# Kernel tuning notes

Hardware: AMD Instinct MI355X
Metric: run time of the kernel (lower is better)

Reference implementation:

```python
import jax, jax.numpy as jnp
import numpy as np

N_NODES = 256


def _lstm_layer(x, W, b):
    # x: [B, T, D]; W: [D+H, 4H]; b: [4H]. TF BasicLSTMCell, forget_bias=1.0,
    # gate order (i, j, f, o).
    B, T, D = x.shape
    H = N_NODES

    def step(carry, xt):
        c, h = carry
        gates = jnp.dot(jnp.concatenate([xt, h], axis=1), W) + b  # [B, 4H]
        i, j, f, o = jnp.split(gates, 4, axis=1)
        c_new = c * jax.nn.sigmoid(f + 1.0) + jax.nn.sigmoid(i) * jnp.tanh(j)
        h_new = jnp.tanh(c_new) * jax.nn.sigmoid(o)
        return (c_new, h_new), h_new

    init = (jnp.zeros((B, H), x.dtype), jnp.zeros((B, H), x.dtype))
    _, ys = jax.lax.scan(step, init, jnp.swapaxes(x, 0, 1))  # ys: [T, B, H]
    return jnp.swapaxes(ys, 0, 1)


def setup_inputs() -> dict:
    key = jax.random.key(0)
    k_x, k_w0, k_w1 = jax.random.split(key, 3)
    B, T, D, H = 32, 2048, 256, N_NODES
    x = jax.random.normal(k_x, (B, T, D), dtype=jnp.float32)
    W0 = jax.random.normal(k_w0, (D + H, 4 * H), dtype=jnp.float32) * 0.05
    b0 = jnp.zeros((4 * H,), dtype=jnp.float32)
    W1 = jax.random.normal(k_w1, (H + H, 4 * H), dtype=jnp.float32) * 0.05
    b1 = jnp.zeros((4 * H,), dtype=jnp.float32)
    return {"x": x, "W0": W0, "b0": b0, "W1": W1, "b1": b1}


def reference(x, W0, b0, W1, b1):
    # 2-layer LSTM stack, zero initial states, keepProb=1.0 (no dropout).
    h = _lstm_layer(x, W0, b0)
    h = _lstm_layer(h, W1, b1)
    # activations = reshape(outputs, [-1, nNodes * numCells]), numCells = 1
    return h.reshape(-1, N_NODES)
```

## Files before the change

### kernel.cpp

```cpp
#include <hip/hip_runtime.h>
#include <hip/hip_bf16.h>
#include <hip/hip_fp16.h>


typedef _Float16 half_t;
typedef __attribute__((ext_vector_type(2))) _Float16 h2v;

static __device__ __forceinline__ float bf2f(unsigned short u) {
  union { unsigned u; float f; } v; v.u = ((unsigned)u) << 16; return v.f;
}
static __device__ __forceinline__ unsigned short f2bf(float f) {
  union { float f; unsigned u; } v; v.f = f;
  unsigned r = v.u + 0x7fffu + ((v.u >> 16) & 1u);
  return (unsigned short)(r >> 16);
}
static __device__ __forceinline__ float ldw(const void* p, long i, int fp32) {
  return fp32 ? ((const float*)p)[i] : bf2f(((const unsigned short*)p)[i]);
}
static __device__ __forceinline__ unsigned short f16b(float f) {
  return __builtin_bit_cast(unsigned short, (half_t)f);
}
static __device__ __forceinline__ h2v BC(unsigned u) {
  return __builtin_bit_cast(h2v, u);
}
static __device__ __forceinline__ float rcpf(float x) { return __builtin_amdgcn_rcpf(x); }
static __device__ __forceinline__ float sigm(float x) { return rcpf(1.f + __expf(-x)); }
static __device__ __forceinline__ float tanh_(float x) {
  float e = __expf(-2.f * fabsf(x));
  float t = (1.f - e) * rcpf(1.f + e);
  return copysignf(t, x);
}
static __device__ __forceinline__ float fdot2(h2v a, h2v b, float c) {
#if __has_builtin(__builtin_amdgcn_fdot2)
  return __builtin_amdgcn_fdot2(a, b, c, false);
#else
  return c + (float)a.x * (float)b.x + (float)a.y * (float)b.y;
#endif
}
static __device__ __forceinline__ unsigned ald(const unsigned* p) {
  return __hip_atomic_load(p, __ATOMIC_RELAXED, __HIP_MEMORY_SCOPE_AGENT);
}
static __device__ __forceinline__ unsigned poll_tag(const unsigned* p, unsigned tg) {
  unsigned v = ald(p);
  while ((v >> 16) != tg) {
    unsigned a = ald(p);
    unsigned b = ald(p);
    unsigned c = ald(p);
    unsigned d = ald(p);
    if ((a >> 16) == tg) { v = a; break; }
    if ((b >> 16) == tg) { v = b; break; }
    if ((c >> 16) == tg) { v = c; break; }
    v = d;
  }
  return v;
}

__global__ __launch_bounds__(256) void detect(const unsigned short* __restrict__ x,
                                              int* __restrict__ flag) {
  __shared__ int cnt;
  if (threadIdx.x == 0) cnt = 0;
  __syncthreads();
  int c = 0;
#pragma unroll
  for (int i = 0; i < 8; ++i) {
    unsigned short u = x[threadIdx.x * 8 + i];
    c += (((u >> 7) & 0xFF) >= 192) ? 1 : 0;
  }
  atomicAdd(&cnt, c);
  __syncthreads();
  if (threadIdx.x == 0) *flag = (cnt > 16) ? 1 : 0;
}

__global__ __launch_bounds__(256) void prep(
    const void* __restrict__ W0, const void* __restrict__ W1,
    const void* __restrict__ b0, const void* __restrict__ b1,
    const int* __restrict__ dtf,
    unsigned* __restrict__ Wrec, float* __restrict__ bias0,
    float* __restrict__ bias1)
{
  const int fp32 = *dtf;
  int id = blockIdx.x * 256 + threadIdx.x;
  if (blockIdx.y == 0) {
    int i  = id & 127;
    int tid = (id >> 7) & 511;
    int sL = id >> 16;
    int L = sL >> 2, s = sL & 3;
    int kq = tid >> 8, c = tid & 255;
    int col = ((c >> 6) << 8) + s * 64 + (c & 63);
    int p  = i >> 6, ii = i & 63;
    long r0 = (long)(p * 256 + kq * 128 + 2 * ii) * 1024 + col;
    const void* W = L ? W1 : W0;
    unsigned lo = f16b(ldw(W, r0, fp32));
    unsigned hi = f16b(ldw(W, r0 + 1024, fp32));
    Wrec[id] = lo | (hi << 16);
  } else {
    if (id < 1024)       bias0[id] = ldw(b0, id, fp32);
    else if (id < 2048)  bias1[id - 1024] = ldw(b1, id - 1024, fp32);
  }
}

__global__ __launch_bounds__(512) void recur(
    const void* __restrict__ x, const unsigned* __restrict__ Wrec,
    const float* __restrict__ bias0, const float* __restrict__ bias1,
    unsigned* H1T, unsigned* H2R,
    void* __restrict__ dout, const int* __restrict__ dtf)
{
  const int fp32 = *dtf;
  const int bi = blockIdx.x;
  const int L = bi >> 7, sL = bi >> 5, s = sL & 3, b = bi & 31;
  const int tid = threadIdx.x;
  const int kq = tid >> 8, c = tid & 255;
  const int abase = kq << 4;
  const int bbase = 32 + (kq << 4);

  __shared__ __align__(16) unsigned short hbufh[512];
  __shared__ float part[2][256];
  __shared__ float bg[256];

  const uint4* wp4 = (const uint4*)Wrec + ((size_t)sL * 512 + tid) * 32;
  uint4 w00 = wp4[0],  w01 = wp4[1],  w02 = wp4[2],  w03 = wp4[3];
  uint4 w04 = wp4[4],  w05 = wp4[5],  w06 = wp4[6],  w07 = wp4[7];
  uint4 w08 = wp4[8],  w09 = wp4[9],  w10 = wp4[10], w11 = wp4[11];
  uint4 w12 = wp4[12], w13 = wp4[13], w14 = wp4[14], w15 = wp4[15];
  uint4 w16 = wp4[16], w17 = wp4[17], w18 = wp4[18], w19 = wp4[19];
  uint4 w20 = wp4[20], w21 = wp4[21], w22 = wp4[22], w23 = wp4[23];
  uint4 w24 = wp4[24], w25 = wp4[25], w26 = wp4[26], w27 = wp4[27];
  uint4 w28 = wp4[28], w29 = wp4[29], w30 = wp4[30], w31 = wp4[31];

  if (tid < 256) {
    int scol = ((c >> 6) << 8) + s * 64 + (c & 63);
    bg[c] = (L ? bias1 : bias0)[scol];
  }

  const uint4* hbufu4 = (const uint4*)hbufh;
  float cst = 0.f;

  float xv = 0.f;
  if (tid < 256) {
    if (!L) {
      size_t xi = (size_t)b * 2048 * 256 + tid;
      hbufh[tid] = f16b(fp32 ? ((const float*)x)[xi]
                             : bf2f(((const unsigned short*)x)[xi]));
      size_t xj = xi + 256;
      xv = fp32 ? ((const float*)x)[xj] : bf2f(((const unsigned short*)x)[xj]);
    } else {
      unsigned v = poll_tag(H1T + (size_t)b * 256 + tid, 0u);
      hbufh[tid] = (unsigned short)v;
    }
  } else {
    hbufh[tid] = 0;
  }
  __syncthreads();

  for (int t = 0; t < 2048; ++t) {
    float a0 = 0.f, a1 = 0.f, a2 = 0.f, a3 = 0.f;
#define STEPD(BASE_, W_, J_) { uint4 hv = hbufu4[BASE_ + J_];  \
    a0 = fdot2(BC(hv.x), BC(W_.x), a0);                        \
    a1 = fdot2(BC(hv.y), BC(W_.y), a1);                        \
    a2 = fdot2(BC(hv.z), BC(W_.z), a2);                        \
    a3 = fdot2(BC(hv.w), BC(W_.w), a3); }
    STEPD(abase, w00, 0)  STEPD(abase, w01, 1)  STEPD(abase, w02, 2)  STEPD(abase, w03, 3)
    STEPD(abase, w04, 4)  STEPD(abase, w05, 5)  STEPD(abase, w06, 6)  STEPD(abase, w07, 7)
    STEPD(abase, w08, 8)  STEPD(abase, w09, 9)  STEPD(abase, w10, 10) STEPD(abase, w11, 11)
    STEPD(abase, w12, 12) STEPD(abase, w13, 13) STEPD(abase, w14, 14) STEPD(abase, w15, 15)

    if (t > 0 && tid >= 256) {
      const unsigned tg = (unsigned)(t - 1);
      const unsigned* pw = L
        ? H2R + ((size_t)((t - 1) & 3) * 32 + b) * 256 + (tid - 256)
        : H1T + ((size_t)(t - 1) * 32 + b) * 256 + (tid - 256);
      hbufh[tid] = (unsigned short)poll_tag(pw, tg);
    }
    __syncthreads();

    STEPD(bbase, w16, 0)  STEPD(bbase, w17, 1)  STEPD(bbase, w18, 2)  STEPD(bbase, w19, 3)
    STEPD(bbase, w20, 4)  STEPD(bbase, w21, 5)  STEPD(bbase, w22, 6)  STEPD(bbase, w23, 7)
    STEPD(bbase, w24, 8)  STEPD(bbase, w25, 9)  STEPD(bbase, w26, 10) STEPD(bbase, w27, 11)
    STEPD(bbase, w28, 12) STEPD(bbase, w29, 13) STEPD(bbase, w30, 14) STEPD(bbase, w31, 15)
#undef STEPD
    part[kq][c] = (a0 + a1) + (a2 + a3);

    if (t < 2047 && tid < 256) {
      if (!L) {
        hbufh[tid] = f16b(xv);
        if (t + 2 < 2048) {
          size_t xi = ((size_t)b * 2048 + (t + 2)) * 256 + tid;
          xv = fp32 ? ((const float*)x)[xi]
                    : bf2f(((const unsigned short*)x)[xi]);
        }
      } else {
        unsigned v = poll_tag(H1T + ((size_t)(t + 1) * 32 + b) * 256 + tid,
                              (unsigned)(t + 1));
        hbufh[tid] = (unsigned short)v;
      }
    }
    __syncthreads();

    if (tid < 64) {
      int j = tid;
      float gi = part[0][j]       + part[1][j]       + bg[j];
      float gj = part[0][64 + j]  + part[1][64 + j]  + bg[64 + j];
      float gf = part[0][128 + j] + part[1][128 + j] + bg[128 + j];
      float go = part[0][192 + j] + part[1][192 + j] + bg[192 + j];
      float cn = cst * sigm(gf + 1.f) + sigm(gi) * tanh_(gj);
      cst = cn;
      float h = tanh_(cn) * sigm(go);
      unsigned val = ((unsigned)t << 16) | (unsigned)f16b(h);
      if (!L) {
        __hip_atomic_store(H1T + ((size_t)t * 32 + b) * 256 + s * 64 + j, val,
                           __ATOMIC_RELAXED, __HIP_MEMORY_SCOPE_AGENT);
      } else {
        __hip_atomic_store(H2R + ((size_t)(t & 3) * 32 + b) * 256 + s * 64 + j,
                           val, __ATOMIC_RELAXED, __HIP_MEMORY_SCOPE_AGENT);
        size_t oi = ((size_t)b * 2048 + t) * 256 + s * 64 + j;
        if (fp32) ((float*)dout)[oi] = h;
        else      ((unsigned short*)dout)[oi] = f2bf(h);
      }
    }
  }
}

extern "C" void kernel_launch(void* const* d_in, const int* in_sizes, int n_in,
                              void* d_out, int out_size, void* d_ws, size_t ws_size,
                              hipStream_t stream) {
  const void* x  = d_in[0];
  const void* W0 = d_in[1];
  const void* b0 = d_in[2];
  const void* W1 = d_in[3];
  const void* b1 = d_in[4];

  char* p = (char*)d_ws;
  unsigned* Wrec = (unsigned*)p; p += (size_t)524288 * 4;
  unsigned* H1T  = (unsigned*)p; p += (size_t)2048 * 32 * 256 * 4;
  unsigned* H2R  = (unsigned*)p; p += (size_t)4 * 32 * 256 * 4;
  float* bias0   = (float*)p;    p += 4096;
  float* bias1   = (float*)p;    p += 4096;
  int* dflag     = (int*)p;      p += 256;

  detect<<<1, 256, 0, stream>>>((const unsigned short*)x, dflag);
  prep<<<dim3(2048, 2), 256, 0, stream>>>(W0, W1, b0, b1, dflag,
                                          Wrec, bias0, bias1);
  recur<<<256, 512, 0, stream>>>(x, Wrec, bias0, bias1,
                                 H1T, H2R, d_out, dflag);
}
```

Baseline: 3.176 ms.

## Poll peer hidden states via L2 CAS probes and keep own slice in LDS

Replaces the relaxed atomic-load polling loop with one that mostly uses a no-op compare-exchange, which forces the read to L2 and so avoids stale cached lines, with a periodic fallback load from a mirror buffer. Each block now writes its own h slice directly into shared memory and skips polling for it. Layer-1 outputs are written twice, once by a volatile store and once by an atomic store to a new mirror array. The goal is lower cross-block handoff latency per timestep, at the cost of extra atomic traffic and store work.

Measured after the change: 4.075 ms. +28.3%, slower.

```diff
diff --git a/kernel.cpp b/kernel.cpp
--- a/kernel.cpp
+++ b/kernel.cpp
@@ -40,19 +40,26 @@
 static __device__ __forceinline__ unsigned ald(const unsigned* p) {
   return __hip_atomic_load(p, __ATOMIC_RELAXED, __HIP_MEMORY_SCOPE_AGENT);
 }
-static __device__ __forceinline__ unsigned poll_tag(const unsigned* p, unsigned tg) {
-  unsigned v = ald(p);
-  while ((v >> 16) != tg) {
-    unsigned a = ald(p);
-    unsigned b = ald(p);
-    unsigned c = ald(p);
-    unsigned d = ald(p);
-    if ((a >> 16) == tg) { v = a; break; }
-    if ((b >> 16) == tg) { v = b; break; }
-    if ((c >> 16) == tg) { v = c; break; }
-    v = d;
-  }
-  return v;
+static __device__ __forceinline__ unsigned l2probe(unsigned* p) {
+  unsigned exp = 0xFFFFFFFFu;
+  __hip_atomic_compare_exchange_strong(p, &exp, 0xFFFFFFFFu,
+                                       __ATOMIC_RELAXED, __ATOMIC_RELAXED,
+                                       __HIP_MEMORY_SCOPE_WORKGROUP);
+  return exp;
+}
+static __device__ __forceinline__ unsigned poll_tag2(const unsigned* fp,
+                                                     const unsigned* sp,
+                                                     unsigned tg) {
+  unsigned* f = (unsigned*)fp;
+  for (;;) {
+#pragma unroll
+    for (int i = 0; i < 4; ++i) {
+      unsigned v = l2probe(f);
+      if ((v >> 16) == tg) return v;
+    }
+    unsigned v = ald(sp);
+    if ((v >> 16) == tg) return v;
+  }
 }
 
 __global__ __launch_bounds__(256) void detect(const unsigned short* __restrict__ x,
@@ -102,7 +109,7 @@
 __global__ __launch_bounds__(512) void recur(
     const void* __restrict__ x, const unsigned* __restrict__ Wrec,
     const float* __restrict__ bias0, const float* __restrict__ bias1,
-    unsigned* H1T, unsigned* H2R,
+    unsigned* H1T, unsigned* H2R, unsigned* H2M,
     void* __restrict__ dout, const int* __restrict__ dtf)
 {
   const int fp32 = *dtf;
@@ -144,8 +151,8 @@
       size_t xj = xi + 256;
       xv = fp32 ? ((const float*)x)[xj] : bf2f(((const unsigned short*)x)[xj]);
     } else {
-      unsigned v = poll_tag(H1T + (size_t)b * 256 + tid, 0u);
-      hbufh[tid] = (unsigned short)v;
+      const unsigned* p0 = H1T + (size_t)b * 256 + tid;
+      hbufh[tid] = (unsigned short)poll_tag2(p0, p0, 0u);
     }
   } else {
     hbufh[tid] = 0;
@@ -165,11 +172,19 @@
     STEPD(abase, w12, 12) STEPD(abase, w13, 13) STEPD(abase, w14, 14) STEPD(abase, w15, 15)
 
     if (t > 0 && tid >= 256) {
-      const unsigned tg = (unsigned)(t - 1);
-      const unsigned* pw = L
-        ? H2R + ((size_t)((t - 1) & 3) * 32 + b) * 256 + (tid - 256)
-        : H1T + ((size_t)(t - 1) * 32 + b) * 256 + (tid - 256);
-      hbufh[tid] = (unsigned short)poll_tag(pw, tg);
+      const int col = tid - 256;
+      if ((col >> 6) != s) {
+        const unsigned tg = (unsigned)(t - 1);
+        unsigned v;
+        if (L) {
+          size_t idx = ((size_t)((t - 1) & 3) * 32 + b) * 256 + col;
+          v = poll_tag2(H2R + idx, H2M + idx, tg);
+        } else {
+          const unsigned* pw = H1T + ((size_t)(t - 1) * 32 + b) * 256 + col;
+          v = poll_tag2(pw, pw, tg);
+        }
+        hbufh[tid] = (unsigned short)v;
+      }
     }
     __syncthreads();
 
@@ -189,9 +204,8 @@
                     : bf2f(((const unsigned short*)x)[xi]);
         }
       } else {
-        unsigned v = poll_tag(H1T + ((size_t)(t + 1) * 32 + b) * 256 + tid,
-                              (unsigned)(t + 1));
-        hbufh[tid] = (unsigned short)v;
+        const unsigned* pw = H1T + ((size_t)(t + 1) * 32 + b) * 256 + tid;
+        hbufh[tid] = (unsigned short)poll_tag2(pw, pw, (unsigned)(t + 1));
       }
     }
     __syncthreads();
@@ -205,13 +219,18 @@
       float cn = cst * sigm(gf + 1.f) + sigm(gi) * tanh_(gj);
       cst = cn;
       float h = tanh_(cn) * sigm(go);
-      unsigned val = ((unsigned)t << 16) | (unsigned)f16b(h);
+      unsigned short hb = f16b(h);
+      unsigned val = ((unsigned)t << 16) | (unsigned)hb;
+      hbufh[256 + (s << 6) + j] = hb;
       if (!L) {
-        __hip_atomic_store(H1T + ((size_t)t * 32 + b) * 256 + s * 64 + j, val,
-                           __ATOMIC_RELAXED, __HIP_MEMORY_SCOPE_AGENT);
+        unsigned* p = H1T + ((size_t)t * 32 + b) * 256 + s * 64 + j;
+        *(volatile unsigned*)p = val;
+        __hip_atomic_store(p, val, __ATOMIC_RELAXED, __HIP_MEMORY_SCOPE_AGENT);
       } else {
-        __hip_atomic_store(H2R + ((size_t)(t & 3) * 32 + b) * 256 + s * 64 + j,
-                           val, __ATOMIC_RELAXED, __HIP_MEMORY_SCOPE_AGENT);
+        size_t idx = ((size_t)(t & 3) * 32 + b) * 256 + s * 64 + j;
+        *(volatile unsigned*)(H2R + idx) = val;
+        __hip_atomic_store(H2M + idx, val, __ATOMIC_RELAXED,
+                           __HIP_MEMORY_SCOPE_AGENT);
         size_t oi = ((size_t)b * 2048 + t) * 256 + s * 64 + j;
         if (fp32) ((float*)dout)[oi] = h;
         else      ((unsigned short*)dout)[oi] = f2bf(h);
@@ -233,6 +252,7 @@
   unsigned* Wrec = (unsigned*)p; p += (size_t)524288 * 4;
   unsigned* H1T  = (unsigned*)p; p += (size_t)2048 * 32 * 256 * 4;
   unsigned* H2R  = (unsigned*)p; p += (size_t)4 * 32 * 256 * 4;
+  unsigned* H2M  = (unsigned*)p; p += (size_t)4 * 32 * 256 * 4;
   float* bias0   = (float*)p;    p += 4096;
   float* bias1   = (float*)p;    p += 4096;
   int* dflag     = (int*)p;      p += 256;
@@ -241,5 +261,5 @@
   prep<<<dim3(2048, 2), 256, 0, stream>>>(W0, W1, b0, b1, dflag,
                                           Wrec, bias0, bias1);
   recur<<<256, 512, 0, stream>>>(x, Wrec, bias0, bias1,
-                                 H1T, H2R, d_out, dflag);
-}
+                                 H1T, H2R, H2M, d_out, dflag);
+}
```

## Interleave two batch rows per block to hide cross-block recurrence latency

Applied to the files above, without the earlier changes.

Each block now handles two batch elements, alternating their timesteps so one element's dot products can run while the other waits on the cross-block hidden-state handoff. This halves the grid to 128 blocks. The block's own slice of h is also written straight into shared memory, so it no longer polls global memory for its own outputs. The cost is roughly double the serial work per block per step and more shared memory, in exchange for overlapping the polling latency.

Measured after the change: 5.050 ms. 1.59x slower.

```diff
diff --git a/kernel.cpp b/kernel.cpp
--- a/kernel.cpp
+++ b/kernel.cpp
@@ -107,14 +107,16 @@
 {
   const int fp32 = *dtf;
   const int bi = blockIdx.x;
-  const int L = bi >> 7, sL = bi >> 5, s = sL & 3, b = bi & 31;
+  const int L = bi >> 6, s = (bi >> 4) & 3, pb = bi & 15;
+  const int b1 = pb, b2 = pb + 16;
+  const int sL = L * 4 + s;
   const int tid = threadIdx.x;
   const int kq = tid >> 8, c = tid & 255;
   const int abase = kq << 4;
   const int bbase = 32 + (kq << 4);
 
-  __shared__ __align__(16) unsigned short hbufh[512];
-  __shared__ float part[2][256];
+  __shared__ __align__(16) unsigned short hbufh[2][512];
+  __shared__ float part[2][2][256];
   __shared__ float bg[256];
 
   const uint4* wp4 = (const uint4*)Wrec + ((size_t)sL * 512 + tid) * 32;
@@ -132,92 +134,115 @@
     bg[c] = (L ? bias1 : bias0)[scol];
   }
 
-  const uint4* hbufu4 = (const uint4*)hbufh;
-  float cst = 0.f;
-
-  float xv = 0.f;
+  float cst1 = 0.f, cst2 = 0.f;
+  float xv1 = 0.f, xv2 = 0.f;
+
   if (tid < 256) {
     if (!L) {
-      size_t xi = (size_t)b * 2048 * 256 + tid;
-      hbufh[tid] = f16b(fp32 ? ((const float*)x)[xi]
-                             : bf2f(((const unsigned short*)x)[xi]));
-      size_t xj = xi + 256;
-      xv = fp32 ? ((const float*)x)[xj] : bf2f(((const unsigned short*)x)[xj]);
+      size_t xi1 = (size_t)b1 * 2048 * 256 + tid;
+      hbufh[0][tid] = f16b(ldw(x, xi1, fp32));
+      xv1 = ldw(x, xi1 + 256, fp32);
+      size_t xi2 = (size_t)b2 * 2048 * 256 + tid;
+      hbufh[1][tid] = f16b(ldw(x, xi2, fp32));
+      xv2 = ldw(x, xi2 + 256, fp32);
     } else {
-      unsigned v = poll_tag(H1T + (size_t)b * 256 + tid, 0u);
-      hbufh[tid] = (unsigned short)v;
+      hbufh[0][tid] = (unsigned short)poll_tag(H1T + (size_t)b1 * 256 + tid, 0u);
+      hbufh[1][tid] = (unsigned short)poll_tag(H1T + (size_t)b2 * 256 + tid, 0u);
     }
   } else {
-    hbufh[tid] = 0;
+    hbufh[0][tid] = 0;
+    hbufh[1][tid] = 0;
   }
   __syncthreads();
 
+#define STEPD(HB_, BASE_, W_, J_) { uint4 hv = HB_[(BASE_) + (J_)];  \
+    a0 = fdot2(BC(hv.x), BC(W_.x), a0);                              \
+    a1 = fdot2(BC(hv.y), BC(W_.y), a1);                              \
+    a2 = fdot2(BC(hv.z), BC(W_.z), a2);                              \
+    a3 = fdot2(BC(hv.w), BC(W_.w), a3); }
+
+#define BSTEP(P_, B_, CST_, XV_) {                                            \
+    const uint4* hb4 = (const uint4*)hbufh[P_];                               \
+    float a0 = 0.f, a1 = 0.f, a2 = 0.f, a3 = 0.f;                             \
+        \
+    STEPD(hb4, abase, w00, 0)  STEPD(hb4, abase, w01, 1)                      \
+    STEPD(hb4, abase, w02, 2)  STEPD(hb4, abase, w03, 3)                      \
+    STEPD(hb4, abase, w04, 4)  STEPD(hb4, abase, w05, 5)                      \
+    STEPD(hb4, abase, w06, 6)  STEPD(hb4, abase, w07, 7)                      \
+    STEPD(hb4, abase, w08, 8)  STEPD(hb4, abase, w09, 9)                      \
+    STEPD(hb4, abase, w10, 10) STEPD(hb4, abase, w11, 11)                     \
+    STEPD(hb4, abase, w12, 12) STEPD(hb4, abase, w13, 13)                     \
+    STEPD(hb4, abase, w14, 14) STEPD(hb4, abase, w15, 15)                     \
+         \
+    if (t > 0 && tid >= 256) {                                                \
+      const int col = tid - 256;                                              \
+      if ((col >> 6) != s) {                                                  \
+        const unsigned tg = (unsigned)(t - 1);                                \
+        const unsigned* pw = L                                                \
+          ? H2R + ((size_t)((t - 1) & 3) * 32 + (B_)) * 256 + col             \
+          : H1T + ((size_t)(t - 1) * 32 + (B_)) * 256 + col;                  \
+        hbufh[P_][tid] = (unsigned short)poll_tag(pw, tg);                    \
+      }                                                                       \
+    }                                                                         \
+    __syncthreads();                                                          \
+              \
+    STEPD(hb4, bbase, w16, 0)  STEPD(hb4, bbase, w17, 1)                      \
+    STEPD(hb4, bbase, w18, 2)  STEPD(hb4, bbase, w19, 3)                      \
+    STEPD(hb4, bbase, w20, 4)  STEPD(hb4, bbase, w21, 5)                      \
+    STEPD(hb4, bbase, w22, 6)  STEPD(hb4, bbase, w23, 7)                      \
+    STEPD(hb4, bbase, w24, 8)  STEPD(hb4, bbase, w25, 9)                      \
+    STEPD(hb4, bbase, w26, 10) STEPD(hb4, bbase, w27, 11)                     \
+    STEPD(hb4, bbase, w28, 12) STEPD(hb4, bbase, w29, 13)                     \
+    STEPD(hb4, bbase, w30, 14) STEPD(hb4, bbase, w31, 15)                     \
+    part[P_][kq][c] = (a0 + a1) + (a2 + a3);                                  \
+                               \
+    if (t < 2047 && tid < 256) {                                              \
+      if (!L) {                                                               \
+        hbufh[P_][tid] = f16b(XV_);                                           \
+        if (t + 2 < 2048) {                                                   \
+          size_t xi = ((size_t)(B_) * 2048 + (t + 2)) * 256 + tid;            \
+          XV_ = ldw(x, xi, fp32);                                             \
+        }                                                                     \
+      } else {                                                                \
+        const unsigned* pw = H1T + ((size_t)(t + 1) * 32 + (B_)) * 256 + tid; \
+        hbufh[P_][tid] = (unsigned short)poll_tag(pw, (unsigned)(t + 1));     \
+      }                                                                       \
+    }                                                                         \
+    __syncthreads();                                                          \
+                 \
+    if (tid < 64) {                                                           \
+      int j = tid;                                                            \
+      float gi = part[P_][0][j]       + part[P_][1][j]       + bg[j];         \
+      float gj = part[P_][0][64 + j]  + part[P_][1][64 + j]  + bg[64 + j];    \
+      float gf = part[P_][0][128 + j] + part[P_][1][128 + j] + bg[128 + j];   \
+      float go = part[P_][0][192 + j] + part[P_][1][192 + j] + bg[192 + j];   \
+      float cn = (CST_) * sigm(gf + 1.f) + sigm(gi) * tanh_(gj);              \
+      CST_ = cn;                                                              \
+      float h = tanh_(cn) * sigm(go);                                         \
+      unsigned short hb = f16b(h);                                            \
+      unsigned val = ((unsigned)t << 16) | (unsigned)hb;                      \
+      hbufh[P_][256 + (s << 6) + j] = hb;                                     \
+      if (!L) {                                                               \
+        __hip_atomic_store(H1T + ((size_t)t * 32 + (B_)) * 256 + s * 64 + j,  \
+                           val, __ATOMIC_RELAXED, __HIP_MEMORY_SCOPE_AGENT);  \
+      } else {                                                                \
+        __hip_atomic_store(                                                   \
+            H2R + ((size_t)(t & 3) * 32 + (B_)) * 256 + s * 64 + j,           \
+            val, __ATOMIC_RELAXED, __HIP_MEMORY_SCOPE_AGENT);                 \
+        size_t oi = ((size_t)(B_) * 2048 + t) * 256 + s * 64 + j;             \
+        if (fp32) ((float*)dout)[oi] = h;                                     \
+        else      ((unsigned short*)dout)[oi] = f2bf(h);                      \
+      }                                                                       \
+    }                                                                         \
+                     \
+  }
+
   for (int t = 0; t < 2048; ++t) {
-    float a0 = 0.f, a1 = 0.f, a2 = 0.f, a3 = 0.f;
-#define STEPD(BASE_, W_, J_) { uint4 hv = hbufu4[BASE_ + J_];  \
-    a0 = fdot2(BC(hv.x), BC(W_.x), a0);                        \
-    a1 = fdot2(BC(hv.y), BC(W_.y), a1);                        \
-    a2 = fdot2(BC(hv.z), BC(W_.z), a2);                        \
-    a3 = fdot2(BC(hv.w), BC(W_.w), a3); }
-    STEPD(abase, w00, 0)  STEPD(abase, w01, 1)  STEPD(abase, w02, 2)  STEPD(abase, w03, 3)
-    STEPD(abase, w04, 4)  STEPD(abase, w05, 5)  STEPD(abase, w06, 6)  STEPD(abase, w07, 7)
-    STEPD(abase, w08, 8)  STEPD(abase, w09, 9)  STEPD(abase, w10, 10) STEPD(abase, w11, 11)
-    STEPD(abase, w12, 12) STEPD(abase, w13, 13) STEPD(abase, w14, 14) STEPD(abase, w15, 15)
-
-    if (t > 0 && tid >= 256) {
-      const unsigned tg = (unsigned)(t - 1);
-      const unsigned* pw = L
-        ? H2R + ((size_t)((t - 1) & 3) * 32 + b) * 256 + (tid - 256)
-        : H1T + ((size_t)(t - 1) * 32 + b) * 256 + (tid - 256);
-      hbufh[tid] = (unsigned short)poll_tag(pw, tg);
-    }
-    __syncthreads();
-
-    STEPD(bbase, w16, 0)  STEPD(bbase, w17, 1)  STEPD(bbase, w18, 2)  STEPD(bbase, w19, 3)
-    STEPD(bbase, w20, 4)  STEPD(bbase, w21, 5)  STEPD(bbase, w22, 6)  STEPD(bbase, w23, 7)
-    STEPD(bbase, w24, 8)  STEPD(bbase, w25, 9)  STEPD(bbase, w26, 10) STEPD(bbase, w27, 11)
-    STEPD(bbase, w28, 12) STEPD(bbase, w29, 13) STEPD(bbase, w30, 14) STEPD(bbase, w31, 15)
+    BSTEP(0, b1, cst1, xv1)
+    BSTEP(1, b2, cst2, xv2)
+  }
+#undef BSTEP
 #undef STEPD
-    part[kq][c] = (a0 + a1) + (a2 + a3);
-
-    if (t < 2047 && tid < 256) {
-      if (!L) {
-        hbufh[tid] = f16b(xv);
-        if (t + 2 < 2048) {
-          size_t xi = ((size_t)b * 2048 + (t + 2)) * 256 + tid;
-          xv = fp32 ? ((const float*)x)[xi]
-                    : bf2f(((const unsigned short*)x)[xi]);
-        }
-      } else {
-        unsigned v = poll_tag(H1T + ((size_t)(t + 1) * 32 + b) * 256 + tid,
-                              (unsigned)(t + 1));
-        hbufh[tid] = (unsigned short)v;
-      }
-    }
-    __syncthreads();
-
-    if (tid < 64) {
-      int j = tid;
-      float gi = part[0][j]       + part[1][j]       + bg[j];
-      float gj = part[0][64 + j]  + part[1][64 + j]  + bg[64 + j];
-      float gf = part[0][128 + j] + part[1][128 + j] + bg[128 + j];
-      float go = part[0][192 + j] + part[1][192 + j] + bg[192 + j];
-      float cn = cst * sigm(gf + 1.f) + sigm(gi) * tanh_(gj);
-      cst = cn;
-      float h = tanh_(cn) * sigm(go);
-      unsigned val = ((unsigned)t << 16) | (unsigned)f16b(h);
-      if (!L) {
-        __hip_atomic_store(H1T + ((size_t)t * 32 + b) * 256 + s * 64 + j, val,
-                           __ATOMIC_RELAXED, __HIP_MEMORY_SCOPE_AGENT);
-      } else {
-        __hip_atomic_store(H2R + ((size_t)(t & 3) * 32 + b) * 256 + s * 64 + j,
-                           val, __ATOMIC_RELAXED, __HIP_MEMORY_SCOPE_AGENT);
-        size_t oi = ((size_t)b * 2048 + t) * 256 + s * 64 + j;
-        if (fp32) ((float*)dout)[oi] = h;
-        else      ((unsigned short*)dout)[oi] = f2bf(h);
-      }
-    }
-  }
 }
 
 extern "C" void kernel_launch(void* const* d_in, const int* in_sizes, int n_in,
@@ -240,6 +265,6 @@
   detect<<<1, 256, 0, stream>>>((const unsigned short*)x, dflag);
   prep<<<dim3(2048, 2), 256, 0, stream>>>(W0, W1, b0, b1, dflag,
                                           Wrec, bias0, bias1);
-  recur<<<256, 512, 0, stream>>>(x, Wrec, bias0, bias1,
+  recur<<<128, 512, 0, stream>>>(x, Wrec, bias0, bias1,
                                  H1T, H2R, d_out, dflag);
 }
```
